# Performance work log

Measured on AMD Instinct MI355X. Metric: run time of the kernel, lower is better.

The kernel has to match this reference:

```python
import jax, jax.numpy as jnp
import numpy as np

B, L, D, H, OUT = 4, 2048, 1024, 8, 256
DH = D // H
EPS = 1e-12


def setup_inputs() -> dict:
    key = jax.random.key(0)
    ks = jax.random.split(key, 20)
    s = lambda fan_in: 1.0 / np.sqrt(fan_in)
    def lin(k, fin, fout):
        k1, k2 = jax.random.split(k)
        w = jax.random.uniform(k1, (fin, fout), jnp.float32, -s(fin), s(fin))
        b = jax.random.uniform(k2, (fout,), jnp.float32, -s(fin), s(fin))
        return w, b
    x = jax.random.normal(ks[0], (B, L, D), jnp.float32)
    wq, bq = lin(ks[1], D, D)
    wk, bk = lin(ks[2], D, D)
    wv, bv = lin(ks[3], D, D)
    gamma = jnp.ones((D,), jnp.float32)
    beta = jnp.zeros((D,), jnp.float32)
    wff, bff = lin(ks[4], D, D)
    wc1, bc1 = lin(ks[5], D, D)
    wc2, bc2 = lin(ks[6], D, 1)
    wl1, bl1 = lin(ks[7], L, L)
    wl2, bl2 = lin(ks[8], L, OUT)
    return dict(x=x, wq=wq, bq=bq, wk=wk, bk=bk, wv=wv, bv=bv,
                gamma=gamma, beta=beta, wff=wff, bff=bff,
                wc1=wc1, bc1=bc1, wc2=wc2, bc2=bc2,
                wl1=wl1, bl1=bl1, wl2=wl2, bl2=bl2)


def layernorm(x, gamma, beta):
    mean = x.mean(-1, keepdims=True)
    var = ((x - mean) ** 2).mean(-1, keepdims=True)  # biased variance
    return gamma * (x - mean) / jnp.sqrt(var + EPS) + beta


def reference(x, wq, bq, wk, bk, wv, bv, gamma, beta, wff, bff,
              wc1, bc1, wc2, bc2, wl1, bl1, wl2, bl2):
    # multi-head self-attention (dropout = identity at inference)
    q = (x @ wq + bq).reshape(B, L, H, DH)
    k = (x @ wk + bk).reshape(B, L, H, DH)
    v = (x @ wv + bv).reshape(B, L, H, DH)
    scores = jnp.einsum('bqhd,bkhd->bhqk', q, k) / np.sqrt(DH)
    attn = jax.nn.softmax(scores, axis=-1)                  # [B,H,L,L]
    ctx = jnp.einsum('bhqk,bkhd->bqhd', attn, v).reshape(B, L, D)
    h = layernorm(x + ctx, gamma, beta)
    # feedforward: Linear + ReLU (hidden = d_model), residual + same layernorm params
    ff = jax.nn.relu(h @ wff + bff)
    h = layernorm(h + ff, gamma, beta)
    # collapse d_model -> 1
    c = jax.nn.relu(h @ wc1 + bc1)
    c = jax.nn.relu(c @ wc2 + bc2)                          # [B,L,1]
    c = jnp.squeeze(c, axis=-1)                             # [B,L]
    # collapse length -> out_featuresize
    c = jax.nn.relu(c @ wl1 + bl1)
    out = c @ wl2 + bl2                                     # [B,OUT]
    return out
```

## Files before the change

kernel.cpp:

```cpp
#include <hip/hip_runtime.h>

typedef unsigned short u16;
typedef unsigned int u32;
typedef __attribute__((ext_vector_type(4))) float f32x4;
typedef __attribute__((ext_vector_type(8))) short short8;
typedef __attribute__((ext_vector_type(4))) u32 u32x4;
typedef __attribute__((ext_vector_type(4))) u16 u16x4;

#define BB 4
#define LL 2048
#define DD 1024
#define HH 8
#define DHH 128

__device__ __forceinline__ u16 f2b(float f) {
  u32 u = __builtin_bit_cast(u32, f);
  u += 0x7fffu + ((u >> 16) & 1u);
  return (u16)(u >> 16);
}
__device__ __forceinline__ float b2f(u16 h) {
  u32 u = ((u32)h) << 16;
  return __builtin_bit_cast(float, u);
}
__device__ __forceinline__ float exp2_fast(float x) {
  float r;
  asm("v_exp_f32 %0, %1" : "=v"(r) : "v"(x));
  return r;
}
__device__ __forceinline__ u32 packbf(float a, float b) {
  return (u32)f2b(a) | ((u32)f2b(b) << 16);
}
__device__ __forceinline__ u32 bperm(int srcLane, u32 v) {
  return (u32)__builtin_amdgcn_ds_bpermute(srcLane << 2, (int)v);
}

#define GLDS16(g, l)                                                          \
  __builtin_amdgcn_global_load_lds(                                           \
      (const __attribute__((address_space(1))) void*)(g),                     \
      (__attribute__((address_space(3))) void*)(l), 16, 0, 0)

__global__ __launch_bounds__(256) void cvt_k(const float* __restrict__ X,
                                             u16* __restrict__ Xb, long n) {
  long i = ((long)blockIdx.x * 256 + threadIdx.x) * 4;
  if (i >= n) return;
  f32x4 v = *(const f32x4*)(X + i);
  u16x4 o;
#pragma unroll
  for (int k = 0; k < 4; k++) o[k] = f2b(v[k]);
  *(u16x4*)(Xb + i) = o;
}

__global__ __launch_bounds__(256) void tr_k(const float* __restrict__ W,
                                            u16* __restrict__ WT) {
  __shared__ float tile[32][33];
  const int bx = blockIdx.x, by = blockIdx.y;
  const int tx = threadIdx.x & 31, ty = threadIdx.x >> 5;
#pragma unroll
  for (int i = 0; i < 4; i++)
    tile[ty + i * 8][tx] =
        W[(long)(by * 32 + ty + i * 8) * 1024 + bx * 32 + tx];
  __syncthreads();
#pragma unroll
  for (int i = 0; i < 4; i++)
    WT[(long)(bx * 32 + ty + i * 8) * 1024 + by * 32 + tx] =
        f2b(tile[tx][ty + i * 8]);
}


__global__ __launch_bounds__(256, 3) void qkv_k(
    const u16* __restrict__ A, const u16* __restrict__ QT,
    const u16* __restrict__ KT, const u16* __restrict__ VTw,
    const float* __restrict__ bq, const float* __restrict__ bk,
    const float* __restrict__ bv, float qscale, u16* __restrict__ Qo,
    u16* __restrict__ Ko, u16* __restrict__ Vo) {
  __shared__ u16 As[2][128 * 32];
  __shared__ u16 Bs[2][128 * 32];
  const int K = 1024;
  const int nwg = gridDim.x * gridDim.y;
  const int bid = blockIdx.x + blockIdx.y * gridDim.x;
  const int swz = (bid & 7) * (nwg >> 3) + (bid >> 3);
  const int bxi = swz % 24, byi = swz / 24;
  const int sector = bxi >> 3;
  const u16* BT = sector == 0 ? QT : (sector == 1 ? KT : VTw);
  const float* bias = sector == 0 ? bq : (sector == 1 ? bk : bv);
  const float scale = sector == 0 ? qscale : 1.f;
  const int t = threadIdx.x;
  const int l = t & 63, w = t >> 6;
  const int lr = l & 15, lg = l >> 4;
  const int wr = (w >> 1) * 64, wc = (w & 1) * 64;
  const long bm = (long)byi * 128, bn = (long)(bxi & 7) * 128;
  const int srow = l >> 2;
  const int scol = (l & 3) * 8;
  const u16* Ag0 = A + (bm + w * 32 + srow) * (long)K + scol;
  const u16* Ag1 = A + (bm + w * 32 + 16 + srow) * (long)K + scol;
  const u16* Bg0 = BT + (bn + w * 32 + srow) * (long)K + scol;
  const u16* Bg1 = BT + (bn + w * 32 + 16 + srow) * (long)K + scol;
  const int wo = w * 1024;
  f32x4 acc[4][4] = {};
  GLDS16(Ag0, &As[0][wo]);
  GLDS16(Ag1, &As[0][wo + 512]);
  GLDS16(Bg0, &Bs[0][wo]);
  GLDS16(Bg1, &Bs[0][wo + 512]);
  __syncthreads();
  int cur = 0;
  for (int k0 = 0; k0 < K; k0 += 32) {
    const int nxt = cur ^ 1;
    if (k0 + 32 < K) {
      GLDS16(Ag0 + k0 + 32, &As[nxt][wo]);
      GLDS16(Ag1 + k0 + 32, &As[nxt][wo + 512]);
      GLDS16(Bg0 + k0 + 32, &Bs[nxt][wo]);
      GLDS16(Bg1 + k0 + 32, &Bs[nxt][wo + 512]);
    }
    short8 af[4], bf[4];
#pragma unroll
    for (int i = 0; i < 4; i++)
      af[i] = *(const short8*)&As[cur][(wr + i * 16 + lr) * 32 + lg * 8];
#pragma unroll
    for (int i = 0; i < 4; i++)
      bf[i] = *(const short8*)&Bs[cur][(wc + i * 16 + lr) * 32 + lg * 8];
#pragma unroll
    for (int i = 0; i < 4; i++)
#pragma unroll
      for (int j = 0; j < 4; j++)
        acc[i][j] = __builtin_amdgcn_mfma_f32_16x16x32_bf16(af[i], bf[j],
                                                            acc[i][j], 0, 0, 0);
    __syncthreads();
    cur = nxt;
  }
#pragma unroll
  for (int i = 0; i < 4; i++)
#pragma unroll
    for (int j = 0; j < 4; j++) {
      long col = bn + wc + j * 16 + lr;
      float bvv = bias[col];
      if (sector == 2) {
        long row0 = bm + wr + i * 16 + lg * 4;
        long b = row0 >> 11, l0 = row0 & 2047;
        u16x4 ov;
#pragma unroll
        for (int r = 0; r < 4; r++) ov[r] = f2b(acc[i][j][r] + bvv);
        *(u16x4*)(Vo + (b * 1024 + col) * 2048 + l0) = ov;
      } else {
        u16* Out = sector == 0 ? Qo : Ko;
#pragma unroll
        for (int r = 0; r < 4; r++) {
          long row = bm + wr + i * 16 + lg * 4 + r;
          Out[row * 1024 + col] = f2b((acc[i][j][r] + bvv) * scale);
        }
      }
    }
}

template <bool RELU, int OMODE>
__global__ __launch_bounds__(256, 3) void gemm_k(
    const u16* __restrict__ A, const u16* __restrict__ BT,
    const float* __restrict__ bias, float scale, float* __restrict__ Cf,
    u16* __restrict__ Cb, int M, int N, int K) {
  __shared__ u16 As[2][128 * 32];
  __shared__ u16 Bs[2][128 * 32];
  const int nwg = gridDim.x * gridDim.y;
  const int bid = blockIdx.x + blockIdx.y * gridDim.x;
  const int swz = (bid & 7) * (nwg >> 3) + (bid >> 3);
  const int bxi = swz % gridDim.x, byi = swz / gridDim.x;
  const int t = threadIdx.x;
  const int l = t & 63, w = t >> 6;
  const int lr = l & 15, lg = l >> 4;
  const int wr = (w >> 1) * 64, wc = (w & 1) * 64;
  const long bm = (long)byi * 128, bn = (long)bxi * 128;
  const int srow = l >> 2;
  const int scol = (l & 3) * 8;
  const u16* Ag0 = A + (bm + w * 32 + srow) * (long)K + scol;
  const u16* Ag1 = A + (bm + w * 32 + 16 + srow) * (long)K + scol;
  const u16* Bg0 = BT + (bn + w * 32 + srow) * (long)K + scol;
  const u16* Bg1 = BT + (bn + w * 32 + 16 + srow) * (long)K + scol;
  const int wo = w * 1024;
  f32x4 acc[4][4] = {};
  GLDS16(Ag0, &As[0][wo]);
  GLDS16(Ag1, &As[0][wo + 512]);
  GLDS16(Bg0, &Bs[0][wo]);
  GLDS16(Bg1, &Bs[0][wo + 512]);
  __syncthreads();
  int cur = 0;
  for (int k0 = 0; k0 < K; k0 += 32) {
    const int nxt = cur ^ 1;
    if (k0 + 32 < K) {
      GLDS16(Ag0 + k0 + 32, &As[nxt][wo]);
      GLDS16(Ag1 + k0 + 32, &As[nxt][wo + 512]);
      GLDS16(Bg0 + k0 + 32, &Bs[nxt][wo]);
      GLDS16(Bg1 + k0 + 32, &Bs[nxt][wo + 512]);
    }
    short8 af[4], bf[4];
#pragma unroll
    for (int i = 0; i < 4; i++)
      af[i] = *(const short8*)&As[cur][(wr + i * 16 + lr) * 32 + lg * 8];
#pragma unroll
    for (int i = 0; i < 4; i++)
      bf[i] = *(const short8*)&Bs[cur][(wc + i * 16 + lr) * 32 + lg * 8];
#pragma unroll
    for (int i = 0; i < 4; i++)
#pragma unroll
      for (int j = 0; j < 4; j++)
        acc[i][j] = __builtin_amdgcn_mfma_f32_16x16x32_bf16(af[i], bf[j],
                                                            acc[i][j], 0, 0, 0);
    __syncthreads();
    cur = nxt;
  }
#pragma unroll
  for (int i = 0; i < 4; i++)
#pragma unroll
    for (int j = 0; j < 4; j++) {
      long col = bn + wc + j * 16 + lr;
      float bv = bias[col];
#pragma unroll
      for (int r = 0; r < 4; r++) {
        long row = bm + wr + i * 16 + lg * 4 + r;
        float v2 = (acc[i][j][r] + bv) * scale;
        if (RELU) v2 = fmaxf(v2, 0.f);
        if (OMODE == 1)
          Cb[row * N + col] = f2b(v2);
        else
          Cf[row * N + col] = v2;
      }
    }
}

__global__ __launch_bounds__(512, 4) void flash_k(const u16* __restrict__ Q,
                                                  const u16* __restrict__ Kb,
                                                  const u16* __restrict__ VT,
                                                  float* __restrict__ ctx) {
  __shared__ u16 Ks2[2][64 * 128];
  __shared__ u16 Vs2[2][128 * 64];
  const int nwg = gridDim.x * gridDim.y;
  const int bid = blockIdx.x + blockIdx.y * gridDim.x;
  const int swz = (bid & 7) * (nwg >> 3) + (bid >> 3);
  const int bxi = swz % gridDim.x, byi = swz / gridDim.x;
  const int t = threadIdx.x;
  const int l = t & 63, w = t >> 6;
  const int lr = l & 15, lg = l >> 4;
  const int b = byi >> 3, h = byi & 7;
  const long kbase = ((long)b * LL) * DD + h * DHH;
  const long vtbase = ((long)(b * 8 + h) * DHH) * LL;
  const int q0 = bxi * 128;

  short8 qf[4];
  {
    const u16* qp = Q + kbase + (long)(q0 + w * 16 + lr) * DD + lg * 8;
#pragma unroll
    for (int c = 0; c < 4; c++) qf[c] = *(const short8*)(qp + c * 32);
  }
  f32x4 oacc[8] = {};
  float mprev = -1e30f;
  float lsum = 0.f;

  const int krA = w * 8 + (l >> 4);
  const int krB = krA + 4;
  const int kc16 = l & 15;
  const int vrA = w * 16 + (l >> 3);
  const int vrB = vrA + 8;
  const int vc16 = l & 7;
  const u16* kg0 = Kb + kbase + (long)krA * DD + (kc16 ^ (krA & 7)) * 8;
  const u16* kg1 = Kb + kbase + (long)krB * DD + (kc16 ^ (krB & 7)) * 8;
  const u16* vg0 = VT + vtbase + (long)vrA * LL + (vc16 ^ (vrA & 7)) * 8;
  const u16* vg1 = VT + vtbase + (long)vrB * LL + (vc16 ^ (vrB & 7)) * 8;
  u16* const kl0 = &Ks2[0][(w * 8) * 128];
  u16* const kl1 = &Ks2[0][(w * 8 + 4) * 128];
  u16* const vl0 = &Vs2[0][(w * 16) * 64];
  u16* const vl1 = &Vs2[0][(w * 16 + 8) * 64];
  GLDS16(kg0, kl0);
  GLDS16(kg1, kl1);
  GLDS16(vg0, vl0);
  GLDS16(vg1, vl1);
  __syncthreads();

  int colk[4], colv[2];
#pragma unroll
  for (int c = 0; c < 4; c++) colk[c] = (((c * 4 + lg) ^ (lr & 7)) * 8);
#pragma unroll
  for (int kk = 0; kk < 2; kk++) colv[kk] = (((kk * 4 + lg) ^ (lr & 7)) * 8);

  const int NT = LL / 64;
  for (int it = 0; it < NT; ++it) {
    const int cur = it & 1;
    if (it + 1 < NT) {
      kg0 += 64 * DD;
      kg1 += 64 * DD;
      vg0 += 64;
      vg1 += 64;
      const int ko = (cur ^ 1) * (64 * 128);
      const int vo = (cur ^ 1) * (128 * 64);
      GLDS16(kg0, kl0 + ko);
      GLDS16(kg1, kl1 + ko);
      GLDS16(vg0, vl0 + vo);
      GLDS16(vg1, vl1 + vo);
    }
    const u16* Kc = &Ks2[cur][0];
    const u16* Vc = &Vs2[cur][0];

    f32x4 s[4] = {};
#pragma unroll
    for (int jc = 0; jc < 4; jc++)
#pragma unroll
      for (int c = 0; c < 4; c++) {
        short8 kf = *(const short8*)&Kc[(jc * 16 + lr) * 128 + colk[c]];
        s[jc] =
            __builtin_amdgcn_mfma_f32_16x16x32_bf16(kf, qf[c], s[jc], 0, 0, 0);
      }

    float mx = fmaxf(fmaxf(s[0][0], s[0][1]), fmaxf(s[0][2], s[0][3]));
#pragma unroll
    for (int jc = 1; jc < 4; jc++)
      mx = fmaxf(mx, fmaxf(fmaxf(s[jc][0], s[jc][1]),
                           fmaxf(s[jc][2], s[jc][3])));
    mx = fmaxf(mx, __shfl_xor(mx, 16, 64));
    mx = fmaxf(mx, __shfl_xor(mx, 32, 64));

    if (__any((int)(mx > mprev + 8.f))) {
      float mn = fmaxf(mprev, mx);
      float alpha = exp2_fast(mprev - mn);
      mprev = mn;
      lsum *= alpha;
      float ar[4];
#pragma unroll
      for (int r = 0; r < 4; r++) ar[r] = __shfl(alpha, lg * 4 + r, 64);
#pragma unroll
      for (int d8 = 0; d8 < 8; d8++)
#pragma unroll
        for (int r = 0; r < 4; r++) oacc[d8][r] *= ar[r];
    }

    u32 pk2[4][2];
    float ladd = 0.f;
#pragma unroll
    for (int jc = 0; jc < 4; jc++) {
      float p0 = exp2_fast(s[jc][0] - mprev);
      float p1 = exp2_fast(s[jc][1] - mprev);
      float p2 = exp2_fast(s[jc][2] - mprev);
      float p3 = exp2_fast(s[jc][3] - mprev);
      ladd += (p0 + p1) + (p2 + p3);
      pk2[jc][0] = packbf(p0, p1);
      pk2[jc][1] = packbf(p2, p3);
    }
    lsum += ladd;

    short8 pf[2];
#pragma unroll
    for (int kk = 0; kk < 2; kk++) {
      u32x4 afv;
#pragma unroll
      for (int m = 0; m < 4; m++) {
        int srcl = lr + ((((lg & 1) << 1) + (m >> 1)) << 4);
        u32 a0 = bperm(srcl, pk2[2 * kk][m & 1]);
        u32 a1 = bperm(srcl, pk2[2 * kk + 1][m & 1]);
        afv[m] = (lg >> 1) ? a1 : a0;
      }
      pf[kk] = __builtin_bit_cast(short8, afv);
    }

#pragma unroll
    for (int kk = 0; kk < 2; kk++)
#pragma unroll
      for (int d8 = 0; d8 < 8; d8++) {
        short8 vf = *(const short8*)&Vc[(d8 * 16 + lr) * 64 + colv[kk]];
        oacc[d8] =
            __builtin_amdgcn_mfma_f32_16x16x32_bf16(pf[kk], vf, oacc[d8], 0,
                                                    0, 0);
      }
    __syncthreads();
  }

  lsum += __shfl_xor(lsum, 16, 64);
  lsum += __shfl_xor(lsum, 32, 64);
#pragma unroll
  for (int r = 0; r < 4; r++) {
    float inv = 1.f / __shfl(lsum, lg * 4 + r, 64);
    float* cp = ctx + kbase + (long)(q0 + w * 16 + lg * 4 + r) * DD;
#pragma unroll
    for (int d8 = 0; d8 < 8; d8++) cp[d8 * 16 + lr] = oacc[d8][r] * inv;
  }
}

__global__ __launch_bounds__(256) void ln_k(const float* __restrict__ X,
                                            const float* __restrict__ R,
                                            const float* __restrict__ gamma,
                                            const float* __restrict__ beta,
                                            float* __restrict__ Hf,
                                            u16* __restrict__ Hb) {
  const int row = blockIdx.x, t = threadIdx.x;
  const long off = (long)row * DD + t * 4;
  f32x4 v = *(const f32x4*)(X + off);
  f32x4 rv = *(const f32x4*)(R + off);
#pragma unroll
  for (int i = 0; i < 4; i++) v[i] += rv[i];
  float s = v[0] + v[1] + v[2] + v[3];
  float q = v[0] * v[0] + v[1] * v[1] + v[2] * v[2] + v[3] * v[3];
#pragma unroll
  for (int m = 32; m >= 1; m >>= 1) {
    s += __shfl_xor(s, m, 64);
    q += __shfl_xor(q, m, 64);
  }
  __shared__ float red[8];
  if ((t & 63) == 0) {
    red[t >> 6] = s;
    red[4 + (t >> 6)] = q;
  }
  __syncthreads();
  s = red[0] + red[1] + red[2] + red[3];
  q = red[4] + red[5] + red[6] + red[7];
  const float mean = s * (1.f / 1024.f);
  const float var = q * (1.f / 1024.f) - mean * mean;
  const float rstd = rsqrtf(var + 1e-12f);
  f32x4 g = *(const f32x4*)(gamma + t * 4);
  f32x4 be = *(const f32x4*)(beta + t * 4);
  f32x4 o;
#pragma unroll
  for (int i = 0; i < 4; i++) o[i] = g[i] * (v[i] - mean) * rstd + be[i];
  if (Hf) *(f32x4*)(Hf + off) = o;
  if (Hb) {
    u16x4 ob;
#pragma unroll
    for (int i = 0; i < 4; i++) ob[i] = f2b(o[i]);
    *(u16x4*)(Hb + off) = ob;
  }
}

__global__ __launch_bounds__(256) void c2_k(const u16* __restrict__ C,
                                            const float* __restrict__ wc2,
                                            const float* __restrict__ bc2,
                                            float* __restrict__ cvec) {
  const int row = blockIdx.x, t = threadIdx.x;
  u16x4 cv = *(const u16x4*)(C + (long)row * DD + t * 4);
  f32x4 wv = *(const f32x4*)(wc2 + t * 4);
  float s = b2f(cv[0]) * wv[0] + b2f(cv[1]) * wv[1] + b2f(cv[2]) * wv[2] +
            b2f(cv[3]) * wv[3];
#pragma unroll
  for (int m = 32; m >= 1; m >>= 1) s += __shfl_xor(s, m, 64);
  __shared__ float red[4];
  if ((t & 63) == 0) red[t >> 6] = s;
  __syncthreads();
  if (t == 0)
    cvec[row] = fmaxf(red[0] + red[1] + red[2] + red[3] + bc2[0], 0.f);
}

__global__ __launch_bounds__(256) void smm_part(const float* __restrict__ Cin,
                                                const float* __restrict__ W,
                                                float* __restrict__ P, int Lr,
                                                int N, int SL) {
  const int j = blockIdx.x * 256 + threadIdx.x;
  const int l0 = blockIdx.y * SL;
  float a0 = 0, a1 = 0, a2 = 0, a3 = 0;
  for (int ll = l0; ll < l0 + SL; ll++) {
    float wv = W[(long)ll * N + j];
    a0 += Cin[ll] * wv;
    a1 += Cin[Lr + ll] * wv;
    a2 += Cin[2 * Lr + ll] * wv;
    a3 += Cin[3 * Lr + ll] * wv;
  }
  float* Pp = P + ((long)blockIdx.y * 4) * N + j;
  Pp[0] = a0;
  Pp[N] = a1;
  Pp[2 * N] = a2;
  Pp[3 * N] = a3;
}

template <bool RELU>
__global__ __launch_bounds__(256) void smm_red(const float* __restrict__ P,
                                               const float* __restrict__ bias,
                                               float* __restrict__ Out, int N,
                                               int S) {
  const int j = blockIdx.x * 256 + threadIdx.x;
#pragma unroll
  for (int b = 0; b < 4; b++) {
    float a = 0;
    for (int s = 0; s < S; s++) a += P[((long)s * 4 + b) * N + j];
    a += bias[j];
    if (RELU) a = fmaxf(a, 0.f);
    Out[(long)b * N + j] = a;
  }
}

extern "C" void kernel_launch(void* const* d_in, const int* in_sizes, int n_in,
                              void* d_out, int out_size, void* d_ws,
                              size_t ws_size, hipStream_t stream) {
  (void)in_sizes; (void)n_in; (void)out_size; (void)ws_size;
  const float* x = (const float*)d_in[0];
  const float* wq = (const float*)d_in[1];
  const float* bq = (const float*)d_in[2];
  const float* wk = (const float*)d_in[3];
  const float* bk = (const float*)d_in[4];
  const float* wv = (const float*)d_in[5];
  const float* bv = (const float*)d_in[6];
  const float* gamma = (const float*)d_in[7];
  const float* beta = (const float*)d_in[8];
  const float* wff = (const float*)d_in[9];
  const float* bff = (const float*)d_in[10];
  const float* wc1 = (const float*)d_in[11];
  const float* bc1 = (const float*)d_in[12];
  const float* wc2 = (const float*)d_in[13];
  const float* bc2 = (const float*)d_in[14];
  const float* wl1 = (const float*)d_in[15];
  const float* bl1 = (const float*)d_in[16];
  const float* wl2 = (const float*)d_in[17];
  const float* bl2 = (const float*)d_in[18];

  char* wsp = (char*)d_ws;
  size_t off = 0;
  auto take = [&](size_t bytes) -> char* {
    char* p = wsp + off;
    off += (bytes + 255) & ~(size_t)255;
    return p;
  };
  u16* xb = (u16*)take((size_t)8192 * 1024 * 2);
  u16* wqT = (u16*)take((size_t)1024 * 1024 * 2);
  u16* wkT = (u16*)take((size_t)1024 * 1024 * 2);
  u16* wvT = (u16*)take((size_t)1024 * 1024 * 2);
  u16* wffT = (u16*)take((size_t)1024 * 1024 * 2);
  u16* wc1T = (u16*)take((size_t)1024 * 1024 * 2);
  u16* qb = (u16*)take((size_t)8192 * 1024 * 2);
  u16* kbuf = (u16*)take((size_t)8192 * 1024 * 2);
  u16* vT = (u16*)take((size_t)8192 * 1024 * 2);
  float* ctxb = (float*)take((size_t)8192 * 1024 * 4);
  float* h1f = (float*)take((size_t)8192 * 1024 * 4);
  float* cvec = (float*)take(8192 * 4);
  float* c3 = (float*)take(8192 * 4);
  float* P1 = (float*)take((size_t)16 * 4 * 2048 * 4);
  float* P2 = (float*)take((size_t)16 * 4 * 256 * 4);
  u16* h1b = qb;
  u16* h2b = kbuf;
  u16* cb = vT;
  float* ff = ctxb;

  cvt_k<<<8192, 256, 0, stream>>>(x, xb, (long)8192 * 1024);
  dim3 trg(32, 32);
  tr_k<<<trg, 256, 0, stream>>>(wq, wqT);
  tr_k<<<trg, 256, 0, stream>>>(wk, wkT);
  tr_k<<<trg, 256, 0, stream>>>(wv, wvT);
  tr_k<<<trg, 256, 0, stream>>>(wff, wffT);
  tr_k<<<trg, 256, 0, stream>>>(wc1, wc1T);

  qkv_k<<<dim3(24, 64), 256, 0, stream>>>(xb, wqT, wkT, wvT, bq, bk, bv,
                                          0.12751743f, qb, kbuf, vT);
  flash_k<<<dim3(16, 32), 512, 0, stream>>>(qb, kbuf, vT, ctxb);
  ln_k<<<8192, 256, 0, stream>>>(x, ctxb, gamma, beta, h1f, h1b);
  dim3 gg(8, 64);
  gemm_k<true, 0><<<gg, 256, 0, stream>>>(h1b, wffT, bff, 1.f, ff, nullptr,
                                          8192, 1024, 1024);
  ln_k<<<8192, 256, 0, stream>>>(h1f, ff, gamma, beta, nullptr, h2b);
  gemm_k<true, 1><<<gg, 256, 0, stream>>>(h2b, wc1T, bc1, 1.f, nullptr, cb,
                                          8192, 1024, 1024);
  c2_k<<<8192, 256, 0, stream>>>(cb, wc2, bc2, cvec);
  smm_part<<<dim3(8, 16), 256, 0, stream>>>(cvec, wl1, P1, 2048, 2048, 128);
  smm_red<true><<<8, 256, 0, stream>>>(P1, bl1, c3, 2048, 16);
  smm_part<<<dim3(1, 16), 256, 0, stream>>>(c3, wl2, P2, 2048, 256, 128);
  smm_red<false><<<1, 256, 0, stream>>>(P2, bl2, (float*)d_out, 256, 16);
}
```

Baseline: 382.2 us.

## Fuse collapse-to-scalar projection into wc1 GEMM epilogue with atomics

The wc1 GEMM epilogue now applies bias and ReLU, multiplies by wc2, reduces across columns with shuffles and atomically adds per-row partials into cvec. The bc2 bias and ReLU move into the first length-collapse kernel. This removes the bf16 write and re-read of the 8192x1024 intermediate and the separate c2 kernel launch, at the cost of a memset and many atomics. The qkv kernel's launch bounds also rise to 4 waves per SIMD, which may force register spills.

```diff
diff --git a/kernel.cpp b/kernel.cpp
--- a/kernel.cpp
+++ b/kernel.cpp
@@ -66,8 +66,7 @@
         f2b(tile[tx][ty + i * 8]);
 }
 
-
-__global__ __launch_bounds__(256, 3) void qkv_k(
+__global__ __launch_bounds__(256, 4) void qkv_k(
     const u16* __restrict__ A, const u16* __restrict__ QT,
     const u16* __restrict__ KT, const u16* __restrict__ VTw,
     const float* __restrict__ bq, const float* __restrict__ bk,
@@ -155,7 +154,8 @@
 __global__ __launch_bounds__(256, 3) void gemm_k(
     const u16* __restrict__ A, const u16* __restrict__ BT,
     const float* __restrict__ bias, float scale, float* __restrict__ Cf,
-    u16* __restrict__ Cb, int M, int N, int K) {
+    u16* __restrict__ Cb, const float* __restrict__ w2,
+    float* __restrict__ cvec, int M, int N, int K) {
   __shared__ u16 As[2][128 * 32];
   __shared__ u16 Bs[2][128 * 32];
   const int nwg = gridDim.x * gridDim.y;
@@ -205,23 +205,47 @@
     __syncthreads();
     cur = nxt;
   }
-#pragma unroll
-  for (int i = 0; i < 4; i++)
+  if (OMODE == 3) {
+    float bvj[4], w2j[4];
 #pragma unroll
     for (int j = 0; j < 4; j++) {
       long col = bn + wc + j * 16 + lr;
-      float bv = bias[col];
+      bvj[j] = bias[col];
+      w2j[j] = w2[col];
+    }
+#pragma unroll
+    for (int i = 0; i < 4; i++)
 #pragma unroll
       for (int r = 0; r < 4; r++) {
-        long row = bm + wr + i * 16 + lg * 4 + r;
-        float v2 = (acc[i][j][r] + bv) * scale;
-        if (RELU) v2 = fmaxf(v2, 0.f);
-        if (OMODE == 1)
-          Cb[row * N + col] = f2b(v2);
-        else
+        float a2 = 0.f;
+#pragma unroll
+        for (int j = 0; j < 4; j++)
+          a2 += fmaxf(acc[i][j][r] + bvj[j], 0.f) * w2j[j];
+        a2 += __shfl_xor(a2, 1, 64);
+        a2 += __shfl_xor(a2, 2, 64);
+        a2 += __shfl_xor(a2, 4, 64);
+        a2 += __shfl_xor(a2, 8, 64);
+        if (lr == 0) {
+          long row = bm + wr + i * 16 + lg * 4 + r;
+          atomicAdd(&cvec[row], a2);
+        }
+      }
+  } else {
+#pragma unroll
+    for (int i = 0; i < 4; i++)
+#pragma unroll
+      for (int j = 0; j < 4; j++) {
+        long col = bn + wc + j * 16 + lr;
+        float bv = bias[col];
+#pragma unroll
+        for (int r = 0; r < 4; r++) {
+          long row = bm + wr + i * 16 + lg * 4 + r;
+          float v2 = (acc[i][j][r] + bv) * scale;
+          if (RELU) v2 = fmaxf(v2, 0.f);
           Cf[row * N + col] = v2;
+        }
       }
-    }
+  }
 }
 
 __global__ __launch_bounds__(512, 4) void flash_k(const u16* __restrict__ Q,
@@ -423,37 +447,30 @@
   }
 }
 
-__global__ __launch_bounds__(256) void c2_k(const u16* __restrict__ C,
-                                            const float* __restrict__ wc2,
-                                            const float* __restrict__ bc2,
-                                            float* __restrict__ cvec) {
-  const int row = blockIdx.x, t = threadIdx.x;
-  u16x4 cv = *(const u16x4*)(C + (long)row * DD + t * 4);
-  f32x4 wv = *(const f32x4*)(wc2 + t * 4);
-  float s = b2f(cv[0]) * wv[0] + b2f(cv[1]) * wv[1] + b2f(cv[2]) * wv[2] +
-            b2f(cv[3]) * wv[3];
-#pragma unroll
-  for (int m = 32; m >= 1; m >>= 1) s += __shfl_xor(s, m, 64);
-  __shared__ float red[4];
-  if ((t & 63) == 0) red[t >> 6] = s;
-  __syncthreads();
-  if (t == 0)
-    cvec[row] = fmaxf(red[0] + red[1] + red[2] + red[3] + bc2[0], 0.f);
-}
-
+template <bool BR>
 __global__ __launch_bounds__(256) void smm_part(const float* __restrict__ Cin,
                                                 const float* __restrict__ W,
                                                 float* __restrict__ P, int Lr,
-                                                int N, int SL) {
+                                                int N, int SL,
+                                                const float* __restrict__ b0) {
   const int j = blockIdx.x * 256 + threadIdx.x;
   const int l0 = blockIdx.y * SL;
+  const float bb = BR ? b0[0] : 0.f;
   float a0 = 0, a1 = 0, a2 = 0, a3 = 0;
   for (int ll = l0; ll < l0 + SL; ll++) {
     float wv = W[(long)ll * N + j];
-    a0 += Cin[ll] * wv;
-    a1 += Cin[Lr + ll] * wv;
-    a2 += Cin[2 * Lr + ll] * wv;
-    a3 += Cin[3 * Lr + ll] * wv;
+    float c0 = Cin[ll], c1 = Cin[Lr + ll], c2 = Cin[2 * Lr + ll],
+          c3 = Cin[3 * Lr + ll];
+    if (BR) {
+      c0 = fmaxf(c0 + bb, 0.f);
+      c1 = fmaxf(c1 + bb, 0.f);
+      c2 = fmaxf(c2 + bb, 0.f);
+      c3 = fmaxf(c3 + bb, 0.f);
+    }
+    a0 += c0 * wv;
+    a1 += c1 * wv;
+    a2 += c2 * wv;
+    a3 += c3 * wv;
   }
   float* Pp = P + ((long)blockIdx.y * 4) * N + j;
   Pp[0] = a0;
@@ -526,7 +543,6 @@
   float* P2 = (float*)take((size_t)16 * 4 * 256 * 4);
   u16* h1b = qb;
   u16* h2b = kbuf;
-  u16* cb = vT;
   float* ff = ctxb;
 
   cvt_k<<<8192, 256, 0, stream>>>(x, xb, (long)8192 * 1024);
@@ -543,13 +559,16 @@
   ln_k<<<8192, 256, 0, stream>>>(x, ctxb, gamma, beta, h1f, h1b);
   dim3 gg(8, 64);
   gemm_k<true, 0><<<gg, 256, 0, stream>>>(h1b, wffT, bff, 1.f, ff, nullptr,
-                                          8192, 1024, 1024);
+                                          nullptr, nullptr, 8192, 1024, 1024);
   ln_k<<<8192, 256, 0, stream>>>(h1f, ff, gamma, beta, nullptr, h2b);
-  gemm_k<true, 1><<<gg, 256, 0, stream>>>(h2b, wc1T, bc1, 1.f, nullptr, cb,
-                                          8192, 1024, 1024);
-  c2_k<<<8192, 256, 0, stream>>>(cb, wc2, bc2, cvec);
-  smm_part<<<dim3(8, 16), 256, 0, stream>>>(cvec, wl1, P1, 2048, 2048, 128);
+  hipMemsetAsync(cvec, 0, 8192 * sizeof(float), stream);
+  gemm_k<true, 3><<<gg, 256, 0, stream>>>(h2b, wc1T, bc1, 1.f, nullptr,
+                                          nullptr, wc2, cvec, 8192, 1024,
+                                          1024);
+  smm_part<true><<<dim3(8, 16), 256, 0, stream>>>(cvec, wl1, P1, 2048, 2048,
+                                                  128, bc2);
   smm_red<true><<<8, 256, 0, stream>>>(P1, bl1, c3, 2048, 16);
-  smm_part<<<dim3(1, 16), 256, 0, stream>>>(c3, wl2, P2, 2048, 256, 128);
+  smm_part<false><<<dim3(1, 16), 256, 0, stream>>>(c3, wl2, P2, 2048, 256,
+                                                   128, nullptr);
   smm_red<false><<<1, 256, 0, stream>>>(P2, bl2, (float*)d_out, 256, 16);
 }
```

Result: no change. 381.2 us (-0.3%).
